# Kernel tuning notes

Measured on AMD Instinct MI355X. Metric: run time of the kernel, lower is better.

Reference implementation:

```python
import jax, jax.numpy as jnp
import numpy as np
from jax import lax

EPS = 1e-8


def _moving_average(x, window):
    # x: [B, T]; replicate-pad left by window-1, then mean-filter (matches F.pad(mode='replicate') + conv1d)
    pad = jnp.repeat(x[:, :1], window - 1, axis=1)
    xp = jnp.concatenate([pad, x], axis=1)[:, None, :]          # [B, 1, T+w-1]
    k = (jnp.ones((1, 1, window), x.dtype) / window)
    out = lax.conv_general_dilated(xp, k, (1,), 'VALID')         # [B, 1, T]
    return out[:, 0, :]


def _ema(x, period):
    # linear recurrence ema[t] = a*x[t] + (1-a)*ema[t-1], ema[0] = x[0]
    alpha = 2.0 / (period + 1)
    def step(carry, xt):
        y = alpha * xt + (1.0 - alpha) * carry
        return y, y
    init = x[:, 0]
    _, ys = lax.scan(step, init, x[:, 1:].T)                     # ys: [T-1, B]
    return jnp.concatenate([x[:, :1], ys.T], axis=1)


def _rsi(close, period=14):
    delta = jnp.diff(close, axis=1, prepend=close[:, :1])
    gain = jnp.where(delta > 0, delta, 0.0)
    loss = jnp.where(delta < 0, -delta, 0.0)
    avg_gain = _moving_average(gain, period)
    avg_loss = _moving_average(loss, period)
    rs = avg_gain / (avg_loss + EPS)
    return 100.0 - 100.0 / (1.0 + rs)


def _macd(close, fast=12, slow=26, signal=9):
    ema_fast = _ema(close, fast)
    ema_slow = _ema(close, slow)
    macd = ema_fast - ema_slow
    signal_line = _ema(macd, signal)
    return macd, signal_line


def _bollinger(close, period=20, num_std=2.0):
    ma = _moving_average(close, period)
    mean = _moving_average(close, period)
    sq_diff = (close - mean) ** 2
    variance = _moving_average(sq_diff, period)
    std = jnp.sqrt(variance + EPS)
    return ma + num_std * std, ma, ma - num_std * std


def _atr(close, period=14):
    high_low = jnp.abs(jnp.diff(close, axis=1, prepend=close[:, :1]))
    return _moving_average(high_low, period)


def _forward(close, volume):
    outs = []
    for window in (5, 10, 20, 50):
        ma = _moving_average(close, window)
        outs.append(ma)
        outs.append(close / (ma + EPS))
    outs.append(_rsi(close, 14))
    macd, signal = _macd(close)
    outs.append(macd)
    outs.append(signal)
    outs.append(macd - signal)
    bb_u, bb_m, bb_l = _bollinger(close, 20)
    outs.append(bb_u)
    outs.append(bb_m)
    outs.append(bb_l)
    outs.append((close - bb_l) / (bb_u - bb_l + EPS))
    outs.append(_atr(close, 14))
    return jnp.stack(outs)                                        # [17, B, T]


def setup_inputs() -> dict:
    key = jax.random.key(0)
    k1, k2 = jax.random.split(key)
    B, T = 512, 8192
    close = jax.random.uniform(k1, (B, T), dtype=jnp.float32)
    volume = jax.random.uniform(k2, (B, T), dtype=jnp.float32)
    return {"close": close, "volume": volume}


def reference(close, volume):
    return _forward(close, volume)
```

## Files before the change

### kernel.cpp

```cpp
#include <hip/hip_runtime.h>
#include <cstddef>

#define NTHREADS 256
#define TROW 8192
#define NROWS 512
#define TILE 1024
#define HALO 256
#define REG 1280
#define CHUNK 5
#define KOUT 4
#define FEPS 1e-8f

static_assert(REG == TILE + HALO, "region");
static_assert(CHUNK * NTHREADS == REG, "chunk");
static_assert(KOUT * NTHREADS == TILE, "kout");

typedef float f32x4 __attribute__((ext_vector_type(4)));

__device__ __forceinline__ float pow_chunk(float b) {
  float b2 = b * b;
  return b2 * b2 * b;
}

__global__ __launch_bounds__(NTHREADS) void feat_kernel(
    const float* __restrict__ close, float* __restrict__ out) {
  __shared__ __align__(16) float cl[REG];
  __shared__ float Qa[REG + 1];
  __shared__ float Qd[REG + 1];
  __shared__ float M[REG];
  __shared__ float Sg[REG];
  __shared__ float sc[24];

  const int tid = threadIdx.x;
  const int lane = tid & 63;
  const int wid = tid >> 6;
  const int j = blockIdx.x;
  const int r = blockIdx.y;
  const int out_start = j * TILE;
  const int s = (j == 0) ? 0 : (out_start - HALO);
  const int ob = out_start - s;
  const size_t BT = (size_t)NROWS * TROW;
  const size_t rbase = (size_t)r * TROW + (size_t)s;

  {
    const f32x4* rp4 = reinterpret_cast<const f32x4*>(close + rbase);
    f32x4* cl4 = reinterpret_cast<f32x4*>(cl);
    cl4[tid] = rp4[tid];
    if (tid < (REG / 4 - NTHREADS)) cl4[NTHREADS + tid] = rp4[NTHREADS + tid];
  }
  __syncthreads();
  const float c0v = cl[0];
  const int c0 = tid * CHUNK;

  const float a12 = 2.f / 13.f, b12 = 11.f / 13.f;
  const float a26 = 2.f / 27.f, b26 = 25.f / 27.f;
  const float a9 = 0.2f, b9 = 0.8f;

  float xk[CHUNK];
  float dk[CHUNK];
  float mreg[CHUNK];

  {
    const float xm1 = (c0 == 0) ? 0.f : cl[c0 - 1];
    float prev = xm1;
    float s_c = 0.f, s_a = 0.f, y1 = 0.f, y2 = 0.f;
#pragma unroll
    for (int k = 0; k < CHUNK; ++k) {
      const int i = c0 + k;
      const float x = cl[i];
      xk[k] = x;
      const float d = (i == 0) ? 0.f : fabsf(x - prev);
      dk[k] = d;
      prev = x;
      s_c += x;
      s_a += d;
      if (i == 0) { y1 = x; y2 = x; }
      else { y1 = fmaf(b12, y1, a12 * x); y2 = fmaf(b26, y2, a26 * x); }
    }
    float xc = s_c, xa = s_a;
    float A1 = (tid == 0) ? 0.f : pow_chunk(b12);
    float A2 = (tid == 0) ? 0.f : pow_chunk(b26);
    float B1 = y1, B2 = y2;
#pragma unroll
    for (int off = 1; off < 64; off <<= 1) {
      const float pc = __shfl_up(xc, off, 64);
      const float pa = __shfl_up(xa, off, 64);
      const float pA1 = __shfl_up(A1, off, 64), pB1 = __shfl_up(B1, off, 64);
      const float pA2 = __shfl_up(A2, off, 64), pB2 = __shfl_up(B2, off, 64);
      if (lane >= off) {
        xc += pc; xa += pa;
        B1 = fmaf(A1, pB1, B1); A1 *= pA1;
        B2 = fmaf(A2, pB2, B2); A2 *= pA2;
      }
    }
    float eA1 = __shfl_up(A1, 1, 64), eB1 = __shfl_up(B1, 1, 64);
    float eA2 = __shfl_up(A2, 1, 64), eB2 = __shfl_up(B2, 1, 64);
    if (lane == 0) { eA1 = 1.f; eB1 = 0.f; eA2 = 1.f; eB2 = 0.f; }
    if (lane == 63) {
      sc[wid * 6 + 0] = xc; sc[wid * 6 + 1] = xa;
      sc[wid * 6 + 2] = A1; sc[wid * 6 + 3] = B1;
      sc[wid * 6 + 4] = A2; sc[wid * 6 + 5] = B2;
    }
    __syncthreads();
    float woc = 0.f, woa = 0.f, cB1 = 0.f, cB2 = 0.f;
    for (int w = 0; w < wid; ++w) {
      woc += sc[w * 6 + 0];
      woa += sc[w * 6 + 1];
      cB1 = fmaf(sc[w * 6 + 2], cB1, sc[w * 6 + 3]);
      cB2 = fmaf(sc[w * 6 + 4], cB2, sc[w * 6 + 5]);
    }
    float rc = woc + xc - s_c;
    float ra = woa + xa - s_a;
    y1 = fmaf(eA1, cB1, eB1);
    y2 = fmaf(eA2, cB2, eB2);
    if (tid == 0) { Qa[0] = 0.f; Qd[0] = 0.f; }
#pragma unroll
    for (int k = 0; k < CHUNK; ++k) {
      const int i = c0 + k;
      const float x = xk[k];
      rc += x;     Qa[i + 1] = rc;
      ra += dk[k]; Qd[i + 1] = ra;
      if (i == 0) { y1 = x; y2 = x; }
      else { y1 = fmaf(b12, y1, a12 * x); y2 = fmaf(b26, y2, a26 * x); }
      const float mm = y1 - y2;
      M[i] = mm;
      mreg[k] = mm;
    }
    __syncthreads();
  }

#pragma unroll
  for (int k = 0; k < KOUT; ++k) {
    const int i = ob + tid + k * NTHREADS;
    const size_t base = rbase + (size_t)i;
    const float c = cl[i];
    const float q1 = Qa[i + 1];
#pragma unroll
    for (int wi = 0; wi < 4; ++wi) {
      const int w = (wi == 0) ? 5 : (wi == 1) ? 10 : (wi == 2) ? 20 : 50;
      const float invw = 1.f / (float)w;
      int al = i + 1 - w;
      float pad = 0.f;
      if (al < 0) { pad = (float)(-al) * c0v; al = 0; }
      const float ma = (q1 - Qa[al] + pad) * invw;
      out[(size_t)(2 * wi) * BT + base] = ma;
      out[(size_t)(2 * wi + 1) * BT + base] = c / (ma + FEPS);
    }
    int ar = i - 13;
    if (ar < 0) ar = 0;
    int ap = ar - 1;
    if (ap < 0) ap = 0;
    const float sabs = Qd[i + 1] - Qd[ar];
    const float sdel = c - cl[ap];
    const float g = (sabs + sdel) * (0.5f / 14.f);
    const float l = (sabs - sdel) * (0.5f / 14.f);
    const float rs = g / (l + FEPS);
    out[8 * BT + base] = 100.f - 100.f / (1.f + rs);
    out[16 * BT + base] = sabs * (1.f / 14.f);
    out[9 * BT + base] = M[i];
  }

  const bool first = (j == 0);
  {
    float vq[CHUNK];
    float s_q = 0.f, y9 = 0.f;
#pragma unroll
    for (int k = 0; k < CHUNK; ++k) {
      const int i = c0 + k;
      float v = 0.f;
      if (first || i >= 19) {
        int al = i - 19;
        float pad = 0.f;
        if (al < 0) { pad = (float)(-al) * c0v; al = 0; }
        const float m20 = (Qa[i + 1] - Qa[al] + pad) * 0.05f;
        const float dd = xk[k] - m20;
        v = dd * dd;
      }
      vq[k] = v;
      s_q += v;
      const float xm = mreg[k];
      if (i == 0) y9 = xm;
      else y9 = fmaf(b9, y9, a9 * xm);
    }
    float xq = s_q;
    float A = (tid == 0) ? 0.f : pow_chunk(b9);
    float Bv = y9;
#pragma unroll
    for (int off = 1; off < 64; off <<= 1) {
      const float pq = __shfl_up(xq, off, 64);
      const float pA = __shfl_up(A, off, 64), pB = __shfl_up(Bv, off, 64);
      if (lane >= off) { xq += pq; Bv = fmaf(A, pB, Bv); A *= pA; }
    }
    float eA = __shfl_up(A, 1, 64), eB = __shfl_up(Bv, 1, 64);
    if (lane == 0) { eA = 1.f; eB = 0.f; }
    if (lane == 63) { sc[wid * 3 + 0] = xq; sc[wid * 3 + 1] = A; sc[wid * 3 + 2] = Bv; }
    __syncthreads();
    float woq = 0.f, cB = 0.f;
    for (int w = 0; w < wid; ++w) {
      woq += sc[w * 3 + 0];
      cB = fmaf(sc[w * 3 + 1], cB, sc[w * 3 + 2]);
    }
    float rq = woq + xq - s_q;
    y9 = fmaf(eA, cB, eB);
    if (tid == 0) Qd[0] = 0.f;
#pragma unroll
    for (int k = 0; k < CHUNK; ++k) {
      const int i = c0 + k;
      rq += vq[k];
      Qd[i + 1] = rq;
      const float xm = mreg[k];
      if (i == 0) y9 = xm;
      else y9 = fmaf(b9, y9, a9 * xm);
      Sg[i] = y9;
    }
    __syncthreads();
  }

#pragma unroll
  for (int k = 0; k < KOUT; ++k) {
    const int i = ob + tid + k * NTHREADS;
    const size_t base = rbase + (size_t)i;
    const float c = cl[i];
    int al = i - 19;
    float pad = 0.f;
    if (al < 0) { pad = (float)(-al) * c0v; al = 0; }
    const float ma20 = (Qa[i + 1] - Qa[al] + pad) * 0.05f;
    int av = i - 19;
    if (av < 0) av = 0;
    float vs = Qd[i + 1] - Qd[av];
    vs = fmaxf(vs, 0.f);
    const float sd = sqrtf(vs * 0.05f + FEPS);
    const float up = ma20 + 2.f * sd;
    const float lo = ma20 - 2.f * sd;
    out[12 * BT + base] = up;
    out[13 * BT + base] = ma20;
    out[14 * BT + base] = lo;
    out[15 * BT + base] = (c - lo) / (up - lo + FEPS);
    const float sg = Sg[i];
    const float m = M[i];
    out[10 * BT + base] = sg;
    out[11 * BT + base] = m - sg;
  }
}

extern "C" void kernel_launch(void* const* d_in, const int* in_sizes, int n_in,
                              void* d_out, int out_size, void* d_ws, size_t ws_size,
                              hipStream_t stream) {
  (void)in_sizes; (void)n_in; (void)out_size; (void)d_ws; (void)ws_size;
  const float* close = (const float*)d_in[0];
  float* out = (float*)d_out;
  dim3 grid(TROW / TILE, NROWS, 1);
  feat_kernel<<<grid, dim3(NTHREADS, 1, 1), 0, stream>>>(close, out);
}
```

Before: 303.0 us.

## Vectorize output stage with float4 LDS loads and global stores using guard padding

Each thread now handles four consecutive output positions instead of four strided ones. Prefix-sum and close buffers get zeroed guard regions, so windowed lookups become aligned float4 LDS reads with no clamping, and all 17 output planes are written with 128-bit global stores. The aim is fewer memory instructions and less index/branch arithmetic in a store-bound kernel. In exchange, shared-memory use grows slightly and the per-thread access pattern changes from coalesced scalar stores to vector stores.

```diff
diff --git a/kernel.cpp b/kernel.cpp
--- a/kernel.cpp
+++ b/kernel.cpp
@@ -8,12 +8,12 @@
 #define HALO 256
 #define REG 1280
 #define CHUNK 5
-#define KOUT 4
+#define GUARD 64
 #define FEPS 1e-8f
 
 static_assert(REG == TILE + HALO, "region");
 static_assert(CHUNK * NTHREADS == REG, "chunk");
-static_assert(KOUT * NTHREADS == TILE, "kout");
+static_assert(4 * NTHREADS == TILE, "ve");
 
 typedef float f32x4 __attribute__((ext_vector_type(4)));
 
@@ -22,14 +22,19 @@
   return b2 * b2 * b;
 }
 
+#define LDV(buf, v) (((const f32x4*)(buf))[(GUARD / 4) + (v)])
+
 __global__ __launch_bounds__(NTHREADS) void feat_kernel(
     const float* __restrict__ close, float* __restrict__ out) {
-  __shared__ __align__(16) float cl[REG];
-  __shared__ float Qa[REG + 1];
-  __shared__ float Qd[REG + 1];
-  __shared__ float M[REG];
-  __shared__ float Sg[REG];
+  __shared__ __align__(16) float QaBuf[GUARD + REG + 4];
+  __shared__ __align__(16) float QdBuf[GUARD + REG + 4];
+  __shared__ __align__(16) float clBuf[GUARD + REG];
+  __shared__ __align__(16) float M[REG];
+  __shared__ __align__(16) float Sg[REG];
   __shared__ float sc[24];
+  float* const Qa = QaBuf + GUARD;
+  float* const Qd = QdBuf + GUARD;
+  float* const cl = clBuf + GUARD;
 
   const int tid = threadIdx.x;
   const int lane = tid & 63;
@@ -41,26 +46,33 @@
   const int ob = out_start - s;
   const size_t BT = (size_t)NROWS * TROW;
   const size_t rbase = (size_t)r * TROW + (size_t)s;
-
-  {
+  const bool first = (j == 0);
+
+  {
+    const f32x4 z = {0.f, 0.f, 0.f, 0.f};
+    if (tid < 16) ((f32x4*)QaBuf)[tid] = z;
+    else if (tid < 32) ((f32x4*)QdBuf)[tid - 16] = z;
+    else if (tid < 48) ((f32x4*)clBuf)[tid - 32] = z;
     const f32x4* rp4 = reinterpret_cast<const f32x4*>(close + rbase);
-    f32x4* cl4 = reinterpret_cast<f32x4*>(cl);
+    f32x4* cl4 = reinterpret_cast<f32x4*>(clBuf) + GUARD / 4;
     cl4[tid] = rp4[tid];
     if (tid < (REG / 4 - NTHREADS)) cl4[NTHREADS + tid] = rp4[NTHREADS + tid];
   }
   __syncthreads();
   const float c0v = cl[0];
   const int c0 = tid * CHUNK;
+  const int i0 = ob + 4 * tid;
+  const int u = i0 >> 2;
 
   const float a12 = 2.f / 13.f, b12 = 11.f / 13.f;
   const float a26 = 2.f / 27.f, b26 = 25.f / 27.f;
   const float a9 = 0.2f, b9 = 0.8f;
 
   float xk[CHUNK];
-  float dk[CHUNK];
   float mreg[CHUNK];
 
   {
+    float dk[CHUNK];
     const float xm1 = (c0 == 0) ? 0.f : cl[c0 - 1];
     float prev = xm1;
     float s_c = 0.f, s_a = 0.f, y1 = 0.f, y2 = 0.f;
@@ -129,38 +141,82 @@
     __syncthreads();
   }
 
-#pragma unroll
-  for (int k = 0; k < KOUT; ++k) {
-    const int i = ob + tid + k * NTHREADS;
-    const size_t base = rbase + (size_t)i;
-    const float c = cl[i];
-    const float q1 = Qa[i + 1];
-#pragma unroll
-    for (int wi = 0; wi < 4; ++wi) {
-      const int w = (wi == 0) ? 5 : (wi == 1) ? 10 : (wi == 2) ? 20 : 50;
-      const float invw = 1.f / (float)w;
-      int al = i + 1 - w;
-      float pad = 0.f;
-      if (al < 0) { pad = (float)(-al) * c0v; al = 0; }
-      const float ma = (q1 - Qa[al] + pad) * invw;
-      out[(size_t)(2 * wi) * BT + base] = ma;
-      out[(size_t)(2 * wi + 1) * BT + base] = c / (ma + FEPS);
-    }
-    int ar = i - 13;
-    if (ar < 0) ar = 0;
-    int ap = ar - 1;
-    if (ap < 0) ap = 0;
-    const float sabs = Qd[i + 1] - Qd[ar];
-    const float sdel = c - cl[ap];
-    const float g = (sabs + sdel) * (0.5f / 14.f);
-    const float l = (sabs - sdel) * (0.5f / 14.f);
-    const float rs = g / (l + FEPS);
-    out[8 * BT + base] = 100.f - 100.f / (1.f + rs);
-    out[16 * BT + base] = sabs * (1.f / 14.f);
-    out[9 * BT + base] = M[i];
-  }
-
-  const bool first = (j == 0);
+  float* const op = out + rbase + (size_t)i0;
+#define ST(f, v) *reinterpret_cast<f32x4*>(op + (size_t)(f) * BT) = (v)
+
+  {
+    const f32x4 a_u  = LDV(QaBuf, u),      a_u1 = LDV(QaBuf, u + 1);
+    const f32x4 a_m1 = LDV(QaBuf, u - 1);
+    const f32x4 a_m3 = LDV(QaBuf, u - 3),  a_m2 = LDV(QaBuf, u - 2);
+    const f32x4 a_m5 = LDV(QaBuf, u - 5),  a_m4 = LDV(QaBuf, u - 4);
+    const f32x4 a_m13 = LDV(QaBuf, u - 13), a_m12 = LDV(QaBuf, u - 12);
+    const f32x4 cv   = LDV(clBuf, u);
+    const float P[4]   = {a_u.y, a_u.z, a_u.w, a_u1.x};
+    const float P5[4]  = {a_m1.x, a_m1.y, a_m1.z, a_m1.w};
+    const float P10[4] = {a_m3.w, a_m2.x, a_m2.y, a_m2.z};
+    const float P20[4] = {a_m5.y, a_m5.z, a_m5.w, a_m4.x};
+    const float P50[4] = {a_m13.w, a_m12.x, a_m12.y, a_m12.z};
+    const float cc[4]  = {cv.x, cv.y, cv.z, cv.w};
+    float pad5[4] = {0, 0, 0, 0}, pad10[4] = {0, 0, 0, 0};
+    float pad20[4] = {0, 0, 0, 0}, pad50[4] = {0, 0, 0, 0};
+    if (first) {
+#pragma unroll
+      for (int k = 0; k < 4; ++k) {
+        const float fi = (float)(i0 + k);
+        pad5[k]  = fmaxf(4.f - fi, 0.f) * c0v;
+        pad10[k] = fmaxf(9.f - fi, 0.f) * c0v;
+        pad20[k] = fmaxf(19.f - fi, 0.f) * c0v;
+        pad50[k] = fmaxf(49.f - fi, 0.f) * c0v;
+      }
+    }
+    f32x4 v0, v1;
+#pragma unroll
+    for (int k = 0; k < 4; ++k) {
+      const float m = (P[k] - P5[k] + pad5[k]) * 0.2f;
+      v0[k] = m; v1[k] = cc[k] / (m + FEPS);
+    }
+    ST(0, v0); ST(1, v1);
+#pragma unroll
+    for (int k = 0; k < 4; ++k) {
+      const float m = (P[k] - P10[k] + pad10[k]) * 0.1f;
+      v0[k] = m; v1[k] = cc[k] / (m + FEPS);
+    }
+    ST(2, v0); ST(3, v1);
+#pragma unroll
+    for (int k = 0; k < 4; ++k) {
+      const float m = (P[k] - P20[k] + pad20[k]) * 0.05f;
+      v0[k] = m; v1[k] = cc[k] / (m + FEPS);
+    }
+    ST(4, v0); ST(5, v1);
+#pragma unroll
+    for (int k = 0; k < 4; ++k) {
+      const float m = (P[k] - P50[k] + pad50[k]) * 0.02f;
+      v0[k] = m; v1[k] = cc[k] / (m + FEPS);
+    }
+    ST(6, v0); ST(7, v1);
+
+    const f32x4 d_u  = LDV(QdBuf, u),     d_u1 = LDV(QdBuf, u + 1);
+    const f32x4 d_m4 = LDV(QdBuf, u - 4), d_m3 = LDV(QdBuf, u - 3);
+    const f32x4 c_m4 = LDV(clBuf, u - 4), c_m3 = LDV(clBuf, u - 3);
+    const float Pd[4]  = {d_u.y, d_u.z, d_u.w, d_u1.x};
+    const float D13[4] = {d_m4.w, d_m3.x, d_m3.y, d_m3.z};
+    const float C14[4] = {c_m4.z, c_m4.w, c_m3.x, c_m3.y};
+#pragma unroll
+    for (int k = 0; k < 4; ++k) {
+      const int i = i0 + k;
+      const float sabs = Pd[k] - D13[k];
+      const float cprev = (i < 14) ? c0v : C14[k];
+      const float sdel = cc[k] - cprev;
+      const float g = (sabs + sdel) * (0.5f / 14.f);
+      const float l = (sabs - sdel) * (0.5f / 14.f);
+      const float rs = g / (l + FEPS);
+      v0[k] = 100.f - 100.f / (1.f + rs);
+      v1[k] = sabs * (1.f / 14.f);
+    }
+    ST(8, v0); ST(16, v1);
+    ST(9, reinterpret_cast<const f32x4*>(M)[u]);
+  }
+
   {
     float vq[CHUNK];
     float s_q = 0.f, y9 = 0.f;
@@ -216,31 +272,42 @@
     __syncthreads();
   }
 
-#pragma unroll
-  for (int k = 0; k < KOUT; ++k) {
-    const int i = ob + tid + k * NTHREADS;
-    const size_t base = rbase + (size_t)i;
-    const float c = cl[i];
-    int al = i - 19;
-    float pad = 0.f;
-    if (al < 0) { pad = (float)(-al) * c0v; al = 0; }
-    const float ma20 = (Qa[i + 1] - Qa[al] + pad) * 0.05f;
-    int av = i - 19;
-    if (av < 0) av = 0;
-    float vs = Qd[i + 1] - Qd[av];
-    vs = fmaxf(vs, 0.f);
-    const float sd = sqrtf(vs * 0.05f + FEPS);
-    const float up = ma20 + 2.f * sd;
-    const float lo = ma20 - 2.f * sd;
-    out[12 * BT + base] = up;
-    out[13 * BT + base] = ma20;
-    out[14 * BT + base] = lo;
-    out[15 * BT + base] = (c - lo) / (up - lo + FEPS);
-    const float sg = Sg[i];
-    const float m = M[i];
-    out[10 * BT + base] = sg;
-    out[11 * BT + base] = m - sg;
-  }
+  {
+    const f32x4 a_u  = LDV(QaBuf, u),     a_u1 = LDV(QaBuf, u + 1);
+    const f32x4 a_m5 = LDV(QaBuf, u - 5), a_m4 = LDV(QaBuf, u - 4);
+    const f32x4 q_u  = LDV(QdBuf, u),     q_u1 = LDV(QdBuf, u + 1);
+    const f32x4 q_m5 = LDV(QdBuf, u - 5), q_m4 = LDV(QdBuf, u - 4);
+    const f32x4 cv   = LDV(clBuf, u);
+    const f32x4 mm = reinterpret_cast<const f32x4*>(M)[u];
+    const f32x4 sg = reinterpret_cast<const f32x4*>(Sg)[u];
+    const float P[4]   = {a_u.y, a_u.z, a_u.w, a_u1.x};
+    const float P20[4] = {a_m5.y, a_m5.z, a_m5.w, a_m4.x};
+    const float Vq[4]  = {q_u.y, q_u.z, q_u.w, q_u1.x};
+    const float V20[4] = {q_m5.y, q_m5.z, q_m5.w, q_m4.x};
+    const float cc[4]  = {cv.x, cv.y, cv.z, cv.w};
+    float pad20[4] = {0, 0, 0, 0};
+    if (first) {
+#pragma unroll
+      for (int k = 0; k < 4; ++k)
+        pad20[k] = fmaxf(19.f - (float)(i0 + k), 0.f) * c0v;
+    }
+    f32x4 up, mid, lo, pb;
+#pragma unroll
+    for (int k = 0; k < 4; ++k) {
+      const float ma20 = (P[k] - P20[k] + pad20[k]) * 0.05f;
+      float vs = Vq[k] - V20[k];
+      vs = fmaxf(vs, 0.f);
+      const float sd = sqrtf(vs * 0.05f + FEPS);
+      up[k] = ma20 + 2.f * sd;
+      mid[k] = ma20;
+      lo[k] = ma20 - 2.f * sd;
+      pb[k] = (cc[k] - lo[k]) / (up[k] - lo[k] + FEPS);
+    }
+    ST(12, up); ST(13, mid); ST(14, lo); ST(15, pb);
+    ST(10, sg);
+    ST(11, mm - sg);
+  }
+#undef ST
 }
 
 extern "C" void kernel_launch(void* const* d_in, const int* in_sizes, int n_in,
```

Result: no change. 305.1 us (+0.7%).
